# Optimization experiments

Measured on AMD Instinct MI355X. Metric: run time of the kernel, lower is better.

## Reference

```python
import jax, jax.numpy as jnp
import numpy as np

N, F, U = 32768, 512, 512
GRID_SIZE, SPLINE_ORDER = 3, 3
GRID_RANGE = (-1.0, 1.0)
LN_EPS = 1e-3  # keras LayerNormalization default epsilon


def _make_grid():
    h = (GRID_RANGE[1] - GRID_RANGE[0]) / GRID_SIZE
    start = -SPLINE_ORDER * h + GRID_RANGE[0]
    stop = (GRID_SIZE + SPLINE_ORDER) * h + GRID_RANGE[0]
    num = GRID_SIZE + 2 * SPLINE_ORDER + 1  # 10 knots
    g = np.linspace(start, stop, num, dtype=np.float32)
    g = np.tile(g, (F, 1))[None, :, :]  # [1, F, num]
    return jnp.asarray(g)


def _glorot(key, shape):
    limit = np.sqrt(6.0 / (shape[0] + shape[1])).astype(np.float32)
    return jax.random.uniform(key, shape, jnp.float32, -limit, limit)


def setup_inputs() -> dict:
    key = jax.random.key(0)
    k_x, k_bw, k_sw = jax.random.split(key, 3)
    return {
        "x": jax.random.normal(k_x, (N, F), jnp.float32),
        "ln_gamma": jnp.ones((F,), jnp.float32),
        "ln_beta": jnp.zeros((F,), jnp.float32),
        "base_weight": _glorot(k_bw, (F, U)),
        "base_bias": jnp.zeros((U,), jnp.float32),
        "spline_weight": _glorot(k_sw, (F * (GRID_SIZE + SPLINE_ORDER), U)),
        "grid": _make_grid(),
    }


def _b_splines(x, grid):
    # x: [N, F]; grid: [1, F, G+2K+1]
    xe = x[..., None]  # [N, F, 1]
    bases = ((xe >= grid[..., :-1]) & (xe < grid[..., 1:])).astype(x.dtype)  # [N,F,G+2K]
    for k in range(1, SPLINE_ORDER + 1):
        left = (xe - grid[..., :-(k + 1)]) / (grid[..., k:-1] - grid[..., :-(k + 1)])
        right = (grid[..., k + 1:] - xe) / (grid[..., k + 1:] - grid[..., 1:-k])
        bases = left * bases[..., :-1] + right * bases[..., 1:]
    return bases.reshape(x.shape[0], -1)  # [N, F*(G+K)]


def reference(x, ln_gamma, ln_beta, base_weight, base_bias, spline_weight, grid):
    # LayerNorm over last axis
    mean = jnp.mean(x, axis=-1, keepdims=True)
    var = jnp.var(x, axis=-1, keepdims=True)
    xn = (x - mean) * jax.lax.rsqrt(var + LN_EPS) * ln_gamma + ln_beta
    # base branch: relu -> matmul -> bias
    base_out = jax.nn.relu(xn) @ base_weight + base_bias
    # spline branch: Cox-de Boor basis -> matmul
    spline_out = _b_splines(xn, grid) @ spline_weight
    # dropout rate 0 / inference -> identity
    return base_out + spline_out
```

## Files before the change

### kernel.cpp

```cpp
#include <hip/hip_runtime.h>
#include <hip/hip_bf16.h>


#define N_ROWS 32768
#define F_DIM  512
#define U_DIM  512
#define K_DIM  4096

typedef short short8 __attribute__((ext_vector_type(8)));
typedef float floatx4 __attribute__((ext_vector_type(4)));

__device__ __forceinline__ float bf2f(unsigned short h) {
    return __uint_as_float(((unsigned int)h) << 16);
}
__device__ __forceinline__ bool probe_bf16(const void* grid) {
    return ((const unsigned int*)grid)[0] != 0xC0400000u;
}
template <bool B16>
__device__ __forceinline__ float ldf(const void* p, int i) {
    return B16 ? bf2f(((const unsigned short*)p)[i]) : ((const float*)p)[i];
}
template <bool B16>
__device__ __forceinline__ void ld4(const void* p, int i, float* o) {
    if (B16) {
        ushort4 v = *(const ushort4*)((const unsigned short*)p + i);
        o[0] = bf2f(v.x); o[1] = bf2f(v.y); o[2] = bf2f(v.z); o[3] = bf2f(v.w);
    } else {
        float4 v = *(const float4*)((const float*)p + i);
        o[0] = v.x; o[1] = v.y; o[2] = v.z; o[3] = v.w;
    }
}
__device__ __forceinline__ unsigned int pk2(float lo, float hi) {
    __hip_bfloat162 h = __float22bfloat162_rn(make_float2(lo, hi));
    return *reinterpret_cast<unsigned int*>(&h);
}

template <bool B16>
__device__ __forceinline__ void ln_stats_body(const void* __restrict__ x,
                                              float2* __restrict__ stats, int bid) {
    int wave = threadIdx.x >> 6, lane = threadIdx.x & 63;
    int row = bid * 4 + wave;
    float v[8];
    ld4<B16>(x, row * F_DIM + lane * 8, v);
    ld4<B16>(x, row * F_DIM + lane * 8 + 4, v + 4);
    float s = 0.f, s2 = 0.f;
#pragma unroll
    for (int k = 0; k < 8; ++k) { s += v[k]; s2 += v[k] * v[k]; }
#pragma unroll
    for (int off = 32; off > 0; off >>= 1) {
        s  += __shfl_xor(s, off);
        s2 += __shfl_xor(s2, off);
    }
    if (lane == 0) {
        float mean = s * (1.0f / F_DIM);
        float var  = s2 * (1.0f / F_DIM) - mean * mean;
        stats[row] = make_float2(mean, rsqrtf(var + 1e-3f));
    }
}
template <bool B16>
__device__ __forceinline__ void build_wt_body(const void* __restrict__ bw,
                                              const void* __restrict__ sw,
                                              unsigned short* __restrict__ wt, int bid) {
    int idx = bid * 256 + threadIdx.x;
    int u = idx & 511;
    int fq = idx >> 9;
#pragma unroll
    for (int i = 0; i < 4; ++i) {
        int f = fq * 4 + i;
        uint4 w;
        w.x = pk2(ldf<B16>(bw, f * U_DIM + u),            ldf<B16>(sw, (f * 6 + 0) * U_DIM + u));
        w.y = pk2(ldf<B16>(sw, (f * 6 + 1) * U_DIM + u),  ldf<B16>(sw, (f * 6 + 2) * U_DIM + u));
        w.z = pk2(ldf<B16>(sw, (f * 6 + 3) * U_DIM + u),  ldf<B16>(sw, (f * 6 + 4) * U_DIM + u));
        w.w = pk2(ldf<B16>(sw, (f * 6 + 5) * U_DIM + u),  0.f);
        *(uint4*)(wt + (size_t)u * K_DIM + f * 8) = w;
    }
}
__global__ __launch_bounds__(256) void prep_k(const void* __restrict__ x,
                                              const void* __restrict__ bw,
                                              const void* __restrict__ sw,
                                              const void* __restrict__ grid,
                                              float2* __restrict__ stats,
                                              unsigned short* __restrict__ wt) {
    int bid = blockIdx.x;
    if (probe_bf16(grid)) {
        if (bid < N_ROWS / 4) ln_stats_body<true>(x, stats, bid);
        else                  build_wt_body<true>(bw, sw, wt, bid - N_ROWS / 4);
    } else {
        if (bid < N_ROWS / 4) ln_stats_body<false>(x, stats, bid);
        else                  build_wt_body<false>(bw, sw, wt, bid - N_ROWS / 4);
    }
}

template <bool B16>
__device__ __forceinline__ uint4 gen_a_pack(const void* __restrict__ x,
                                            const void* __restrict__ gam,
                                            const void* __restrict__ bet,
                                            int xrow, int f, float mean, float rstd) {
    float xv = ldf<B16>(x, xrow + f);
    float gv = ldf<B16>(gam, f);
    float bv = ldf<B16>(bet, f);
    float xn = fmaf(xv - mean, rstd * gv, bv);
    float tt = fmaf(xn, 1.5f, 4.5f);
    float bb[6];
#pragma unroll
    for (int j = 0; j < 6; ++j) {
        float d = tt - (float)(j + 2);
        float a = fabsf(d);
        float a2 = d * d;
        float v1 = fmaf(fmaf(0.5f, a, -1.0f), a2, 0.66666669f);
        float c = fmaxf(2.0f - a, 0.0f);
        float v2 = c * c * c * (1.0f / 6.0f);
        bb[j] = (a < 1.0f) ? v1 : v2;
    }
    uint4 o;
    o.x = pk2(fmaxf(xn, 0.f), bb[0]);
    o.y = pk2(bb[1], bb[2]);
    o.z = pk2(bb[3], bb[4]);
    o.w = pk2(bb[5], 0.f);
    return o;
}

template <bool B16>
__device__ __forceinline__ void kan_gemm_body(
    const void* __restrict__ x,
    const float2* __restrict__ stats,
    const unsigned short* __restrict__ wt,
    const void* __restrict__ gam,
    const void* __restrict__ bet,
    const void* __restrict__ bias,
    void* __restrict__ out) {
    __shared__ __align__(16) unsigned short Alds[2][128 * 32];
    __shared__ __align__(16) unsigned short Blds[2][2048 * 8];

    const int tid = threadIdx.x;
    const int lane = tid & 63, wv = tid >> 6;
    const int rtile = blockIdx.x;

    const int arow = tid & 127, fg = tid >> 7;
    const int grow = rtile * 128 + arow;
    const float2 st = stats[grow];
    const float mean = st.x, rstd = st.y;
    const int xrow = grow * F_DIM;
    const int aslot = ((arow >> 4) * 4 + fg) * 16 + (arow & 15);

    const unsigned short* gsrc[4];
#pragma unroll
    for (int i = 0; i < 4; ++i) {
        int s = wv * 256 + i * 64 + lane;
        int C = ((s >> 6) << 4) | (s & 15);
        int q = (s >> 4) & 3;
        gsrc[i] = wt + (size_t)C * K_DIM + q * 8;
    }
    const int bbase = (wv * 256) * 8;

    const int wr = wv >> 2, wc = wv & 3;
    const int lr = lane & 15, lq = lane >> 4;

    floatx4 acc[4][8];
#pragma unroll
    for (int mi = 0; mi < 4; ++mi)
#pragma unroll
        for (int ni = 0; ni < 8; ++ni) acc[mi][ni] = (floatx4){0.f, 0.f, 0.f, 0.f};

#pragma unroll
    for (int i = 0; i < 4; ++i)
        __builtin_amdgcn_global_load_lds(
            (const __attribute__((address_space(1))) void*)gsrc[i],
            (__attribute__((address_space(3))) void*)&Blds[0][bbase + i * 64 * 8], 16, 0, 0);
    {
        uint4 p0 = gen_a_pack<B16>(x, gam, bet, xrow, fg, mean, rstd);
        *(uint4*)&Alds[0][aslot * 8] = p0;
    }
    __syncthreads();

    for (int ks = 0; ks < K_DIM / 32 - 1; ++ks) {
        const int cur = ks & 1, nxt = cur ^ 1;

#pragma unroll
        for (int i = 0; i < 4; ++i)
            __builtin_amdgcn_global_load_lds(
                (const __attribute__((address_space(1))) void*)(gsrc[i] + (ks + 1) * 32),
                (__attribute__((address_space(3))) void*)&Blds[nxt][bbase + i * 64 * 8], 16, 0, 0);

        short8 afr[4], bfr[8];
#pragma unroll
        for (int mi = 0; mi < 4; ++mi)
            afr[mi] = *(const short8*)&Alds[cur][((wr * 4 + mi) * 64 + lane) * 8];
#pragma unroll
        for (int ni = 0; ni < 8; ++ni)
            bfr[ni] = *(const short8*)&Blds[cur][((wc * 8 + ni) * 64 + lane) * 8];

        uint4 pkv = gen_a_pack<B16>(x, gam, bet, xrow, (ks + 1) * 4 + fg, mean, rstd);
        *(uint4*)&Alds[nxt][aslot * 8] = pkv;

#pragma unroll
        for (int mi = 0; mi < 4; ++mi)
#pragma unroll
            for (int ni = 0; ni < 8; ++ni)
                acc[mi][ni] = __builtin_amdgcn_mfma_f32_16x16x32_bf16(
                    afr[mi], bfr[ni], acc[mi][ni], 0, 0, 0);

        __syncthreads();
    }

    {
        short8 afr[4], bfr[8];
#pragma unroll
        for (int mi = 0; mi < 4; ++mi)
            afr[mi] = *(const short8*)&Alds[1][((wr * 4 + mi) * 64 + lane) * 8];
#pragma unroll
        for (int ni = 0; ni < 8; ++ni)
            bfr[ni] = *(const short8*)&Blds[1][((wc * 8 + ni) * 64 + lane) * 8];
#pragma unroll
        for (int mi = 0; mi < 4; ++mi)
#pragma unroll
            for (int ni = 0; ni < 8; ++ni)
                acc[mi][ni] = __builtin_amdgcn_mfma_f32_16x16x32_bf16(
                    afr[mi], bfr[ni], acc[mi][ni], 0, 0, 0);
    }

    float biasv[8];
#pragma unroll
    for (int ni = 0; ni < 8; ++ni)
        biasv[ni] = ldf<B16>(bias, wc * 128 + ni * 16 + lr);
#pragma unroll
    for (int mi = 0; mi < 4; ++mi)
#pragma unroll
        for (int ni = 0; ni < 8; ++ni)
#pragma unroll
            for (int r = 0; r < 4; ++r) {
                int row = rtile * 128 + wr * 64 + mi * 16 + lq * 4 + r;
                int col = wc * 128 + ni * 16 + lr;
                float val = acc[mi][ni][r] + biasv[ni];
                if (B16) ((unsigned short*)out)[(size_t)row * U_DIM + col] =
                    (unsigned short)(pk2(val, 0.f) & 0xffffu);
                else ((float*)out)[(size_t)row * U_DIM + col] = val;
            }
}
__global__ __launch_bounds__(512, 2) void kan_gemm(
    const void* __restrict__ x, const float2* __restrict__ stats,
    const unsigned short* __restrict__ wt, const void* __restrict__ gam,
    const void* __restrict__ bet, const void* __restrict__ bias,
    const void* __restrict__ grid, void* __restrict__ out) {
    if (probe_bf16(grid)) kan_gemm_body<true>(x, stats, wt, gam, bet, bias, out);
    else                  kan_gemm_body<false>(x, stats, wt, gam, bet, bias, out);
}

extern "C" void kernel_launch(void* const* d_in, const int* in_sizes, int n_in,
                              void* d_out, int out_size, void* d_ws, size_t ws_size,
                              hipStream_t stream) {
    const void* x    = d_in[0];
    const void* gam  = d_in[1];
    const void* bet  = d_in[2];
    const void* bw   = d_in[3];
    const void* bb   = d_in[4];
    const void* sw   = d_in[5];
    const void* grid = d_in[6];

    float2* stats = (float2*)d_ws;
    unsigned short* wt = (unsigned short*)((char*)d_ws + N_ROWS * sizeof(float2));

    hipLaunchKernelGGL(prep_k, dim3(N_ROWS / 4 + U_DIM * 128 / 256), dim3(256), 0, stream,
                       x, bw, sw, grid, stats, wt);
    hipLaunchKernelGGL(kan_gemm, dim3(N_ROWS / 128), dim3(512), 0, stream,
                       x, stats, wt, gam, bet, bb, grid, d_out);
}
```

Baseline: 356.2 us.

## Shrink GEMM row tile to 64 rows with 4 waves per block

Changes the fused LayerNorm/B-spline GEMM from a 128-row tile with 8 waves (2x4 wave grid) to a 64-row tile with 4 waves, each covering all 64 rows and 128 output columns. Each thread now loads 8 weight chunks per k-step instead of 4 and generates one A pack per k-step, keyed by its row and quad. The grid doubles to 512 blocks, which is meant to improve scheduling and fill across the GPU's compute units. In exchange, each weight tile is reused across half as many rows, so traffic for the 4 MB bf16 weight matrix doubles, and the per-block loads now fall on fewer threads.

Result: slower. 439.6 us (+23.4%).

```diff
diff --git a/kernel.cpp b/kernel.cpp
--- a/kernel.cpp
+++ b/kernel.cpp
@@ -128,32 +128,31 @@
     const void* __restrict__ gam,
     const void* __restrict__ bet,
     const void* __restrict__ bias,
-    void* __restrict__ out) {
-    __shared__ __align__(16) unsigned short Alds[2][128 * 32];
-    __shared__ __align__(16) unsigned short Blds[2][2048 * 8];
+    void* __restrict__ out,
+    unsigned short* __restrict__ Alds,
+    unsigned short* __restrict__ Blds) {
 
     const int tid = threadIdx.x;
     const int lane = tid & 63, wv = tid >> 6;
     const int rtile = blockIdx.x;
 
-    const int arow = tid & 127, fg = tid >> 7;
-    const int grow = rtile * 128 + arow;
+    const int ar = ((tid >> 6) << 4) | (tid & 15);
+    const int aq = (tid >> 4) & 3;
+    const int grow = rtile * 64 + ar;
     const float2 st = stats[grow];
     const float mean = st.x, rstd = st.y;
     const int xrow = grow * F_DIM;
-    const int aslot = ((arow >> 4) * 4 + fg) * 16 + (arow & 15);
-
-    const unsigned short* gsrc[4];
-#pragma unroll
-    for (int i = 0; i < 4; ++i) {
-        int s = wv * 256 + i * 64 + lane;
+
+    const unsigned short* gsrc[8];
+#pragma unroll
+    for (int i = 0; i < 8; ++i) {
+        int s = wv * 512 + i * 64 + lane;
         int C = ((s >> 6) << 4) | (s & 15);
         int q = (s >> 4) & 3;
         gsrc[i] = wt + (size_t)C * K_DIM + q * 8;
     }
-    const int bbase = (wv * 256) * 8;
-
-    const int wr = wv >> 2, wc = wv & 3;
+    const int bbase = wv * 512 * 8;
+
     const int lr = lane & 15, lq = lane >> 4;
 
     floatx4 acc[4][8];
@@ -163,35 +162,39 @@
         for (int ni = 0; ni < 8; ++ni) acc[mi][ni] = (floatx4){0.f, 0.f, 0.f, 0.f};
 
 #pragma unroll
-    for (int i = 0; i < 4; ++i)
+    for (int i = 0; i < 8; ++i)
         __builtin_amdgcn_global_load_lds(
             (const __attribute__((address_space(1))) void*)gsrc[i],
-            (__attribute__((address_space(3))) void*)&Blds[0][bbase + i * 64 * 8], 16, 0, 0);
+            (__attribute__((address_space(3))) void*)&Blds[bbase + i * 64 * 8], 16, 0, 0);
     {
-        uint4 p0 = gen_a_pack<B16>(x, gam, bet, xrow, fg, mean, rstd);
-        *(uint4*)&Alds[0][aslot * 8] = p0;
+        uint4 p0 = gen_a_pack<B16>(x, gam, bet, xrow, aq, mean, rstd);
+        *(uint4*)&Alds[tid * 8] = p0;
     }
     __syncthreads();
 
     for (int ks = 0; ks < K_DIM / 32 - 1; ++ks) {
         const int cur = ks & 1, nxt = cur ^ 1;
-
-#pragma unroll
-        for (int i = 0; i < 4; ++i)
+        unsigned short* __restrict__ Ac = Alds + cur * 2048;
+        unsigned short* __restrict__ An = Alds + nxt * 2048;
+        unsigned short* __restrict__ Bc = Blds + cur * 16384;
+        unsigned short* __restrict__ Bn = Blds + nxt * 16384;
+
+#pragma unroll
+        for (int i = 0; i < 8; ++i)
             __builtin_amdgcn_global_load_lds(
                 (const __attribute__((address_space(1))) void*)(gsrc[i] + (ks + 1) * 32),
-                (__attribute__((address_space(3))) void*)&Blds[nxt][bbase + i * 64 * 8], 16, 0, 0);
+                (__attribute__((address_space(3))) void*)&Bn[bbase + i * 64 * 8], 16, 0, 0);
 
         short8 afr[4], bfr[8];
 #pragma unroll
         for (int mi = 0; mi < 4; ++mi)
-            afr[mi] = *(const short8*)&Alds[cur][((wr * 4 + mi) * 64 + lane) * 8];
+            afr[mi] = *(const short8*)&Ac[(mi * 64 + lane) * 8];
 #pragma unroll
         for (int ni = 0; ni < 8; ++ni)
-            bfr[ni] = *(const short8*)&Blds[cur][((wc * 8 + ni) * 64 + lane) * 8];
-
-        uint4 pkv = gen_a_pack<B16>(x, gam, bet, xrow, (ks + 1) * 4 + fg, mean, rstd);
-        *(uint4*)&Alds[nxt][aslot * 8] = pkv;
+            bfr[ni] = *(const short8*)&Bc[((wv * 8 + ni) * 64 + lane) * 8];
+
+        uint4 pkv = gen_a_pack<B16>(x, gam, bet, xrow, (ks + 1) * 4 + aq, mean, rstd);
+        *(uint4*)&An[tid * 8] = pkv;
 
 #pragma unroll
         for (int mi = 0; mi < 4; ++mi)
@@ -204,13 +207,15 @@
     }
 
     {
+        const unsigned short* Ac = Alds + 2048;
+        const unsigned short* Bc = Blds + 16384;
         short8 afr[4], bfr[8];
 #pragma unroll
         for (int mi = 0; mi < 4; ++mi)
-            afr[mi] = *(const short8*)&Alds[1][((wr * 4 + mi) * 64 + lane) * 8];
+            afr[mi] = *(const short8*)&Ac[(mi * 64 + lane) * 8];
 #pragma unroll
         for (int ni = 0; ni < 8; ++ni)
-            bfr[ni] = *(const short8*)&Blds[1][((wc * 8 + ni) * 64 + lane) * 8];
+            bfr[ni] = *(const short8*)&Bc[((wv * 8 + ni) * 64 + lane) * 8];
 #pragma unroll
         for (int mi = 0; mi < 4; ++mi)
 #pragma unroll
@@ -222,28 +227,30 @@
     float biasv[8];
 #pragma unroll
     for (int ni = 0; ni < 8; ++ni)
-        biasv[ni] = ldf<B16>(bias, wc * 128 + ni * 16 + lr);
+        biasv[ni] = ldf<B16>(bias, wv * 128 + ni * 16 + lr);
 #pragma unroll
     for (int mi = 0; mi < 4; ++mi)
 #pragma unroll
         for (int ni = 0; ni < 8; ++ni)
 #pragma unroll
             for (int r = 0; r < 4; ++r) {
-                int row = rtile * 128 + wr * 64 + mi * 16 + lq * 4 + r;
-                int col = wc * 128 + ni * 16 + lr;
+                int row = rtile * 64 + mi * 16 + lq * 4 + r;
+                int col = wv * 128 + ni * 16 + lr;
                 float val = acc[mi][ni][r] + biasv[ni];
                 if (B16) ((unsigned short*)out)[(size_t)row * U_DIM + col] =
                     (unsigned short)(pk2(val, 0.f) & 0xffffu);
                 else ((float*)out)[(size_t)row * U_DIM + col] = val;
             }
 }
-__global__ __launch_bounds__(512, 2) void kan_gemm(
+__global__ __launch_bounds__(256, 2) void kan_gemm(
     const void* __restrict__ x, const float2* __restrict__ stats,
     const unsigned short* __restrict__ wt, const void* __restrict__ gam,
     const void* __restrict__ bet, const void* __restrict__ bias,
     const void* __restrict__ grid, void* __restrict__ out) {
-    if (probe_bf16(grid)) kan_gemm_body<true>(x, stats, wt, gam, bet, bias, out);
-    else                  kan_gemm_body<false>(x, stats, wt, gam, bet, bias, out);
+    __shared__ __align__(16) unsigned short Alds[2 * 2048];
+    __shared__ __align__(16) unsigned short Blds[2 * 16384];
+    if (probe_bf16(grid)) kan_gemm_body<true>(x, stats, wt, gam, bet, bias, out, Alds, Blds);
+    else                  kan_gemm_body<false>(x, stats, wt, gam, bet, bias, out, Alds, Blds);
 }
 
 extern "C" void kernel_launch(void* const* d_in, const int* in_sizes, int n_in,
@@ -262,6 +269,6 @@
 
     hipLaunchKernelGGL(prep_k, dim3(N_ROWS / 4 + U_DIM * 128 / 256), dim3(256), 0, stream,
                        x, bw, sw, grid, stats, wt);
-    hipLaunchKernelGGL(kan_gemm, dim3(N_ROWS / 128), dim3(512), 0, stream,
+    hipLaunchKernelGGL(kan_gemm, dim3(N_ROWS / 64), dim3(256), 0, stream,
                        x, stats, wt, gam, bet, bb, grid, d_out);
 }
```

## Fuse LayerNorm stats into GEMM, amortize A-tile generation across two k-steps

Applied to the files above, without the earlier changes.

Moves the per-row LayerNorm mean/rstd computation out of the prep kernel and into the GEMM block, which reduces each row tile from global memory before the main loop and keeps the stats in LDS. Gamma and beta are cached in LDS. The A tile now covers 8 features (two k-steps) per buffer, and the x values for future steps are prefetched into registers two groups ahead. MFMA sections are wrapped with s_setprio. This removes the stats round-trip through global memory and part of the prep launch work, at the cost of an extra read of x per block and more LDS use, which may lower occupancy.

New measurement: 331.7 us. 1.07x faster.

```diff
diff --git a/kernel.cpp b/kernel.cpp
--- a/kernel.cpp
+++ b/kernel.cpp
@@ -8,6 +8,7 @@
 #define K_DIM  4096
 
 typedef short short8 __attribute__((ext_vector_type(8)));
+typedef unsigned short ushort8v __attribute__((ext_vector_type(8)));
 typedef float floatx4 __attribute__((ext_vector_type(4)));
 
 __device__ __forceinline__ float bf2f(unsigned short h) {
@@ -21,42 +22,26 @@
     return B16 ? bf2f(((const unsigned short*)p)[i]) : ((const float*)p)[i];
 }
 template <bool B16>
-__device__ __forceinline__ void ld4(const void* p, int i, float* o) {
+__device__ __forceinline__ void ld8f(const void* p, int i, float* o) {
     if (B16) {
-        ushort4 v = *(const ushort4*)((const unsigned short*)p + i);
-        o[0] = bf2f(v.x); o[1] = bf2f(v.y); o[2] = bf2f(v.z); o[3] = bf2f(v.w);
+        ushort8v v = *(const ushort8v*)((const unsigned short*)p + i);
+#pragma unroll
+        for (int k = 0; k < 8; ++k) o[k] = bf2f(v[k]);
     } else {
-        float4 v = *(const float4*)((const float*)p + i);
-        o[0] = v.x; o[1] = v.y; o[2] = v.z; o[3] = v.w;
+        float4 a = *(const float4*)((const float*)p + i);
+        float4 b = *(const float4*)((const float*)p + i + 4);
+        o[0]=a.x; o[1]=a.y; o[2]=a.z; o[3]=a.w; o[4]=b.x; o[5]=b.y; o[6]=b.z; o[7]=b.w;
     }
 }
 __device__ __forceinline__ unsigned int pk2(float lo, float hi) {
     __hip_bfloat162 h = __float22bfloat162_rn(make_float2(lo, hi));
     return *reinterpret_cast<unsigned int*>(&h);
 }
-
-template <bool B16>
-__device__ __forceinline__ void ln_stats_body(const void* __restrict__ x,
-                                              float2* __restrict__ stats, int bid) {
-    int wave = threadIdx.x >> 6, lane = threadIdx.x & 63;
-    int row = bid * 4 + wave;
-    float v[8];
-    ld4<B16>(x, row * F_DIM + lane * 8, v);
-    ld4<B16>(x, row * F_DIM + lane * 8 + 4, v + 4);
-    float s = 0.f, s2 = 0.f;
-#pragma unroll
-    for (int k = 0; k < 8; ++k) { s += v[k]; s2 += v[k] * v[k]; }
-#pragma unroll
-    for (int off = 32; off > 0; off >>= 1) {
-        s  += __shfl_xor(s, off);
-        s2 += __shfl_xor(s2, off);
-    }
-    if (lane == 0) {
-        float mean = s * (1.0f / F_DIM);
-        float var  = s2 * (1.0f / F_DIM) - mean * mean;
-        stats[row] = make_float2(mean, rsqrtf(var + 1e-3f));
-    }
-}
+__device__ __forceinline__ void gld_lds16(const unsigned short* g, unsigned short* l) {
+    __builtin_amdgcn_global_load_lds((const __attribute__((address_space(1))) void*)g,
+                                     (__attribute__((address_space(3))) void*)l, 16, 0, 0);
+}
+
 template <bool B16>
 __device__ __forceinline__ void build_wt_body(const void* __restrict__ bw,
                                               const void* __restrict__ sw,
@@ -75,30 +60,16 @@
         *(uint4*)(wt + (size_t)u * K_DIM + f * 8) = w;
     }
 }
-__global__ __launch_bounds__(256) void prep_k(const void* __restrict__ x,
-                                              const void* __restrict__ bw,
+__global__ __launch_bounds__(256) void prep_k(const void* __restrict__ bw,
                                               const void* __restrict__ sw,
                                               const void* __restrict__ grid,
-                                              float2* __restrict__ stats,
                                               unsigned short* __restrict__ wt) {
-    int bid = blockIdx.x;
-    if (probe_bf16(grid)) {
-        if (bid < N_ROWS / 4) ln_stats_body<true>(x, stats, bid);
-        else                  build_wt_body<true>(bw, sw, wt, bid - N_ROWS / 4);
-    } else {
-        if (bid < N_ROWS / 4) ln_stats_body<false>(x, stats, bid);
-        else                  build_wt_body<false>(bw, sw, wt, bid - N_ROWS / 4);
-    }
-}
-
-template <bool B16>
-__device__ __forceinline__ uint4 gen_a_pack(const void* __restrict__ x,
-                                            const void* __restrict__ gam,
-                                            const void* __restrict__ bet,
-                                            int xrow, int f, float mean, float rstd) {
-    float xv = ldf<B16>(x, xrow + f);
-    float gv = ldf<B16>(gam, f);
-    float bv = ldf<B16>(bet, f);
+    if (probe_bf16(grid)) build_wt_body<true>(bw, sw, wt, blockIdx.x);
+    else                  build_wt_body<false>(bw, sw, wt, blockIdx.x);
+}
+
+__device__ __forceinline__ uint4 spline_pack(float xv, float gv, float bv,
+                                             float mean, float rstd) {
     float xn = fmaf(xv - mean, rstd * gv, bv);
     float tt = fmaf(xn, 1.5f, 4.5f);
     float bb[6];
@@ -123,25 +94,43 @@
 template <bool B16>
 __device__ __forceinline__ void kan_gemm_body(
     const void* __restrict__ x,
-    const float2* __restrict__ stats,
     const unsigned short* __restrict__ wt,
     const void* __restrict__ gam,
     const void* __restrict__ bet,
     const void* __restrict__ bias,
-    void* __restrict__ out) {
-    __shared__ __align__(16) unsigned short Alds[2][128 * 32];
-    __shared__ __align__(16) unsigned short Blds[2][2048 * 8];
+    void* __restrict__ out,
+    unsigned short* __restrict__ Alds,
+    unsigned short* __restrict__ Blds,
+    float2* __restrict__ gb,
+    float2* __restrict__ st) {
 
     const int tid = threadIdx.x;
     const int lane = tid & 63, wv = tid >> 6;
     const int rtile = blockIdx.x;
-
-    const int arow = tid & 127, fg = tid >> 7;
-    const int grow = rtile * 128 + arow;
-    const float2 st = stats[grow];
-    const float mean = st.x, rstd = st.y;
-    const int xrow = grow * F_DIM;
-    const int aslot = ((arow >> 4) * 4 + fg) * 16 + (arow & 15);
+    const int lr = lane & 15, lq = lane >> 4;
+    const int wr = wv >> 2, wc = wv & 3;
+
+    gb[tid] = make_float2(ldf<B16>(gam, tid), ldf<B16>(bet, tid));
+
+    {
+        const int row = tid >> 2, sub = tid & 3;
+        const int base = (rtile * 128 + row) * F_DIM + sub * 128;
+        float s = 0.f, s2 = 0.f;
+#pragma unroll
+        for (int i = 0; i < 16; ++i) {
+            float v[8];
+            ld8f<B16>(x, base + i * 8, v);
+#pragma unroll
+            for (int k = 0; k < 8; ++k) { s += v[k]; s2 += v[k] * v[k]; }
+        }
+        s += __shfl_xor(s, 1); s2 += __shfl_xor(s2, 1);
+        s += __shfl_xor(s, 2); s2 += __shfl_xor(s2, 2);
+        if (sub == 0) {
+            float mean = s * (1.0f / F_DIM);
+            float var  = s2 * (1.0f / F_DIM) - mean * mean;
+            st[row] = make_float2(mean, rsqrtf(var + 1e-3f));
+        }
+    }
 
     const unsigned short* gsrc[4];
 #pragma unroll
@@ -151,10 +140,37 @@
         int q = (s >> 4) & 3;
         gsrc[i] = wt + (size_t)C * K_DIM + q * 8;
     }
-    const int bbase = (wv * 256) * 8;
-
-    const int wr = wv >> 2, wc = wv & 3;
-    const int lr = lane & 15, lq = lane >> 4;
+#pragma unroll
+    for (int i = 0; i < 4; ++i)
+        gld_lds16(gsrc[i], &Blds[wv * 2048 + i * 512]);
+
+    __syncthreads();
+
+    const int ar = tid & 127, w = tid >> 7;
+    const float2 ms = st[ar];
+    const float mean = ms.x, rstd = ms.y;
+    const int xrow = (rtile * 128 + ar) * F_DIM;
+    const int aoff = (ar >> 4) * 512 + w * 128 + (ar & 15) * 8;
+
+    {
+        float x0 = ldf<B16>(x, xrow + w);
+        float x1 = ldf<B16>(x, xrow + 4 + w);
+        float2 ga = gb[w], gc = gb[4 + w];
+        *(uint4*)&Alds[aoff]        = spline_pack(x0, ga.x, ga.y, mean, rstd);
+        *(uint4*)&Alds[4096 + aoff] = spline_pack(x1, gc.x, gc.y, mean, rstd);
+    }
+    unsigned short xu0, xu1; float xf0, xf1;
+    if (B16) {
+        xu0 = ((const unsigned short*)x)[xrow + 8 + w];
+        xu1 = ((const unsigned short*)x)[xrow + 12 + w];
+    } else {
+        xf0 = ((const float*)x)[xrow + 8 + w];
+        xf1 = ((const float*)x)[xrow + 12 + w];
+    }
+    __syncthreads();
+    float xC[2];
+    if (B16) { xC[0] = bf2f(xu0); xC[1] = bf2f(xu1); }
+    else     { xC[0] = xf0;       xC[1] = xf1; }
 
     floatx4 acc[4][8];
 #pragma unroll
@@ -162,61 +178,57 @@
 #pragma unroll
         for (int ni = 0; ni < 8; ++ni) acc[mi][ni] = (floatx4){0.f, 0.f, 0.f, 0.f};
 
-#pragma unroll
-    for (int i = 0; i < 4; ++i)
-        __builtin_amdgcn_global_load_lds(
-            (const __attribute__((address_space(1))) void*)gsrc[i],
-            (__attribute__((address_space(3))) void*)&Blds[0][bbase + i * 64 * 8], 16, 0, 0);
-    {
-        uint4 p0 = gen_a_pack<B16>(x, gam, bet, xrow, fg, mean, rstd);
-        *(uint4*)&Alds[0][aslot * 8] = p0;
-    }
-    __syncthreads();
-
-    for (int ks = 0; ks < K_DIM / 32 - 1; ++ks) {
-        const int cur = ks & 1, nxt = cur ^ 1;
-
-#pragma unroll
-        for (int i = 0; i < 4; ++i)
-            __builtin_amdgcn_global_load_lds(
-                (const __attribute__((address_space(1))) void*)(gsrc[i] + (ks + 1) * 32),
-                (__attribute__((address_space(3))) void*)&Blds[nxt][bbase + i * 64 * 8], 16, 0, 0);
-
-        short8 afr[4], bfr[8];
-#pragma unroll
-        for (int mi = 0; mi < 4; ++mi)
-            afr[mi] = *(const short8*)&Alds[cur][((wr * 4 + mi) * 64 + lane) * 8];
-#pragma unroll
-        for (int ni = 0; ni < 8; ++ni)
-            bfr[ni] = *(const short8*)&Blds[cur][((wc * 8 + ni) * 64 + lane) * 8];
-
-        uint4 pkv = gen_a_pack<B16>(x, gam, bet, xrow, (ks + 1) * 4 + fg, mean, rstd);
-        *(uint4*)&Alds[nxt][aslot * 8] = pkv;
-
-#pragma unroll
-        for (int mi = 0; mi < 4; ++mi)
+    for (int g = 0; g < 64; ++g) {
+        unsigned short* __restrict__ Ac = Alds + (g & 1) * 8192;
+        unsigned short* __restrict__ An = Alds + ((g & 1) ^ 1) * 8192;
+        if (g < 62) {
+            int fx = (g + 2) * 8 + w;
+            if (B16) {
+                xu0 = ((const unsigned short*)x)[xrow + fx];
+                xu1 = ((const unsigned short*)x)[xrow + fx + 4];
+            } else {
+                xf0 = ((const float*)x)[xrow + fx];
+                xf1 = ((const float*)x)[xrow + fx + 4];
+            }
+        }
+        const bool dogen = (g < 63);
+        const int f0n = (g + 1) * 8 + w;
+#pragma unroll
+        for (int p = 0; p < 2; ++p) {
+            const int ks = g * 2 + p;
+            unsigned short* __restrict__ Bc = Blds + (ks & 1) * 16384;
+            unsigned short* __restrict__ Bn = Blds + ((ks & 1) ^ 1) * 16384;
+            if (ks < 127) {
+#pragma unroll
+                for (int i = 0; i < 4; ++i)
+                    gld_lds16(gsrc[i] + (ks + 1) * 32, &Bn[wv * 2048 + i * 512]);
+            }
+            short8 afr[4], bfr[8];
+#pragma unroll
+            for (int mi = 0; mi < 4; ++mi)
+                afr[mi] = *(const short8*)&Ac[p * 4096 + ((wr * 4 + mi) * 64 + lane) * 8];
 #pragma unroll
             for (int ni = 0; ni < 8; ++ni)
-                acc[mi][ni] = __builtin_amdgcn_mfma_f32_16x16x32_bf16(
-                    afr[mi], bfr[ni], acc[mi][ni], 0, 0, 0);
-
-        __syncthreads();
-    }
-
-    {
-        short8 afr[4], bfr[8];
-#pragma unroll
-        for (int mi = 0; mi < 4; ++mi)
-            afr[mi] = *(const short8*)&Alds[1][((wr * 4 + mi) * 64 + lane) * 8];
-#pragma unroll
-        for (int ni = 0; ni < 8; ++ni)
-            bfr[ni] = *(const short8*)&Blds[1][((wc * 8 + ni) * 64 + lane) * 8];
-#pragma unroll
-        for (int mi = 0; mi < 4; ++mi)
-#pragma unroll
-            for (int ni = 0; ni < 8; ++ni)
-                acc[mi][ni] = __builtin_amdgcn_mfma_f32_16x16x32_bf16(
-                    afr[mi], bfr[ni], acc[mi][ni], 0, 0, 0);
+                bfr[ni] = *(const short8*)&Bc[((wc * 8 + ni) * 64 + lane) * 8];
+            if (dogen) {
+                float2 g2 = gb[f0n + 4 * p];
+                *(uint4*)&An[p * 4096 + aoff] =
+                    spline_pack(xC[p], g2.x, g2.y, mean, rstd);
+            }
+            __builtin_amdgcn_s_setprio(1);
+#pragma unroll
+            for (int mi = 0; mi < 4; ++mi)
+#pragma unroll
+                for (int ni = 0; ni < 8; ++ni)
+                    acc[mi][ni] = __builtin_amdgcn_mfma_f32_16x16x32_bf16(
+                        afr[mi], bfr[ni], acc[mi][ni], 0, 0, 0);
+            __builtin_amdgcn_s_setprio(0);
+            __syncthreads();
+        }
+        if (g < 62) {
+            if (B16) { xC[0] = bf2f(xu0); xC[1] = bf2f(xu1); }
+            else     { xC[0] = xf0;       xC[1] = xf1; }
+        }
     }
 
     float biasv[8];
@@ -238,12 +250,18 @@
             }
 }
 __global__ __launch_bounds__(512, 2) void kan_gemm(
-    const void* __restrict__ x, const float2* __restrict__ stats,
-    const unsigned short* __restrict__ wt, const void* __restrict__ gam,
-    const void* __restrict__ bet, const void* __restrict__ bias,
-    const void* __restrict__ grid, void* __restrict__ out) {
-    if (probe_bf16(grid)) kan_gemm_body<true>(x, stats, wt, gam, bet, bias, out);
-    else                  kan_gemm_body<false>(x, stats, wt, gam, bet, bias, out);
+    const void* __restrict__ x, const unsigned short* __restrict__ wt,
+    const void* __restrict__ gam, const void* __restrict__ bet,
+    const void* __restrict__ bias, const void* __restrict__ grid,
+    void* __restrict__ out) {
+    __shared__ __align__(16) unsigned short Alds[2 * 8192];
+    __shared__ __align__(16) unsigned short Blds[2 * 16384];
+    __shared__ float2 gb_lds[512];
+    __shared__ float2 st_lds[128];
+    if (probe_bf16(grid))
+        kan_gemm_body<true>(x, wt, gam, bet, bias, out, Alds, Blds, gb_lds, st_lds);
+    else
+        kan_gemm_body<false>(x, wt, gam, bet, bias, out, Alds, Blds, gb_lds, st_lds);
 }
 
 extern "C" void kernel_launch(void* const* d_in, const int* in_sizes, int n_in,
@@ -257,11 +275,10 @@
     const void* sw   = d_in[5];
     const void* grid = d_in[6];
 
-    float2* stats = (float2*)d_ws;
-    unsigned short* wt = (unsigned short*)((char*)d_ws + N_ROWS * sizeof(float2));
-
-    hipLaunchKernelGGL(prep_k, dim3(N_ROWS / 4 + U_DIM * 128 / 256), dim3(256), 0, stream,
-                       x, bw, sw, grid, stats, wt);
+    unsigned short* wt = (unsigned short*)d_ws;
+
+    hipLaunchKernelGGL(prep_k, dim3(U_DIM * 128 / 256), dim3(256), 0, stream,
+                       bw, sw, grid, wt);
     hipLaunchKernelGGL(kan_gemm, dim3(N_ROWS / 128), dim3(512), 0, stream,
-                       x, stats, wt, gam, bet, bb, grid, d_out);
-}
+                       x, wt, gam, bet, bb, grid, d_out);
+}
```

## Split GEMM into 64x256 tiles with 2D grid, LDS gamma/beta, setprio

Applied to the files above, without the earlier changes.

Shrinks the per-block output tile from 128x512 to 64x256 using 256-thread blocks on a 2D grid, targeting three blocks per CU for more latency hiding. Gamma/beta are cached in LDS as float2 and MFMA sections are wrapped in s_setprio. The trade-off is duplicated spline basis generation across column tiles, more B-weight traffic, and fewer MFMAs per LDS fragment read.

Result: slower. 444.2 us (+24.7%).

```diff
diff --git a/kernel.cpp b/kernel.cpp
--- a/kernel.cpp
+++ b/kernel.cpp
@@ -8,6 +8,7 @@
 #define K_DIM  4096
 
 typedef short short8 __attribute__((ext_vector_type(8)));
+typedef unsigned short ushort8v __attribute__((ext_vector_type(8)));
 typedef float floatx4 __attribute__((ext_vector_type(4)));
 
 __device__ __forceinline__ float bf2f(unsigned short h) {
@@ -21,7 +22,7 @@
     return B16 ? bf2f(((const unsigned short*)p)[i]) : ((const float*)p)[i];
 }
 template <bool B16>
-__device__ __forceinline__ void ld4(const void* p, int i, float* o) {
+__device__ __forceinline__ void ld4v(const void* p, int i, float* o) {
     if (B16) {
         ushort4 v = *(const ushort4*)((const unsigned short*)p + i);
         o[0] = bf2f(v.x); o[1] = bf2f(v.y); o[2] = bf2f(v.z); o[3] = bf2f(v.w);
@@ -34,6 +35,10 @@
     __hip_bfloat162 h = __float22bfloat162_rn(make_float2(lo, hi));
     return *reinterpret_cast<unsigned int*>(&h);
 }
+__device__ __forceinline__ void gld_lds16(const unsigned short* g, unsigned short* l) {
+    __builtin_amdgcn_global_load_lds((const __attribute__((address_space(1))) void*)g,
+                                     (__attribute__((address_space(3))) void*)l, 16, 0, 0);
+}
 
 template <bool B16>
 __device__ __forceinline__ void ln_stats_body(const void* __restrict__ x,
@@ -41,8 +46,8 @@
     int wave = threadIdx.x >> 6, lane = threadIdx.x & 63;
     int row = bid * 4 + wave;
     float v[8];
-    ld4<B16>(x, row * F_DIM + lane * 8, v);
-    ld4<B16>(x, row * F_DIM + lane * 8 + 4, v + 4);
+    ld4v<B16>(x, row * F_DIM + lane * 8, v);
+    ld4v<B16>(x, row * F_DIM + lane * 8 + 4, v + 4);
     float s = 0.f, s2 = 0.f;
 #pragma unroll
     for (int k = 0; k < 8; ++k) { s += v[k]; s2 += v[k] * v[k]; }
@@ -91,14 +96,8 @@
     }
 }
 
-template <bool B16>
-__device__ __forceinline__ uint4 gen_a_pack(const void* __restrict__ x,
-                                            const void* __restrict__ gam,
-                                            const void* __restrict__ bet,
-                                            int xrow, int f, float mean, float rstd) {
-    float xv = ldf<B16>(x, xrow + f);
-    float gv = ldf<B16>(gam, f);
-    float bv = ldf<B16>(bet, f);
+__device__ __forceinline__ uint4 spline_pack(float xv, float gv, float bv,
+                                             float mean, float rstd) {
     float xn = fmaf(xv - mean, rstd * gv, bv);
     float tt = fmaf(xn, 1.5f, 4.5f);
     float bb[6];
@@ -128,20 +127,27 @@
     const void* __restrict__ gam,
     const void* __restrict__ bet,
     const void* __restrict__ bias,
-    void* __restrict__ out) {
-    __shared__ __align__(16) unsigned short Alds[2][128 * 32];
-    __shared__ __align__(16) unsigned short Blds[2][2048 * 8];
+    void* __restrict__ out,
+    unsigned short* __restrict__ Alds,
+    unsigned short* __restrict__ Blds,
+    float2* __restrict__ gb) {
 
     const int tid = threadIdx.x;
     const int lane = tid & 63, wv = tid >> 6;
-    const int rtile = blockIdx.x;
-
-    const int arow = tid & 127, fg = tid >> 7;
-    const int grow = rtile * 128 + arow;
+    const int ctile = blockIdx.x;
+    const int rtile = blockIdx.y;
+    const int lr = lane & 15, lq = lane >> 4;
+    const int wr = wv >> 1, wc = wv & 1;
+
+    gb[tid]       = make_float2(ldf<B16>(gam, tid),       ldf<B16>(bet, tid));
+    gb[tid + 256] = make_float2(ldf<B16>(gam, tid + 256), ldf<B16>(bet, tid + 256));
+
+    const int ar = tid >> 2, fg = tid & 3;
+    const int grow = rtile * 64 + ar;
     const float2 st = stats[grow];
     const float mean = st.x, rstd = st.y;
     const int xrow = grow * F_DIM;
-    const int aslot = ((arow >> 4) * 4 + fg) * 16 + (arow & 15);
+    const int aoff = (((ar >> 4) * 4 + fg) * 16 + (ar & 15)) * 8;
 
     const unsigned short* gsrc[4];
 #pragma unroll
@@ -149,70 +155,73 @@
         int s = wv * 256 + i * 64 + lane;
         int C = ((s >> 6) << 4) | (s & 15);
         int q = (s >> 4) & 3;
-        gsrc[i] = wt + (size_t)C * K_DIM + q * 8;
-    }
-    const int bbase = (wv * 256) * 8;
-
-    const int wr = wv >> 2, wc = wv & 3;
-    const int lr = lane & 15, lq = lane >> 4;
-
-    floatx4 acc[4][8];
-#pragma unroll
-    for (int mi = 0; mi < 4; ++mi)
+        gsrc[i] = wt + (size_t)(ctile * 256 + C) * K_DIM + q * 8;
+    }
+
+#pragma unroll
+    for (int i = 0; i < 4; ++i)
+        gld_lds16(gsrc[i], &Blds[(wv * 256 + i * 64) * 8]);
+    {
+        float xv = ldf<B16>(x, xrow + fg);
+        float gv = ldf<B16>(gam, fg), bv = ldf<B16>(bet, fg);
+        *(uint4*)&Alds[aoff] = spline_pack(xv, gv, bv, mean, rstd);
+    }
+    __syncthreads();
+
+    floatx4 acc[2][8];
+#pragma unroll
+    for (int mi = 0; mi < 2; ++mi)
 #pragma unroll
         for (int ni = 0; ni < 8; ++ni) acc[mi][ni] = (floatx4){0.f, 0.f, 0.f, 0.f};
-
-#pragma unroll
-    for (int i = 0; i < 4; ++i)
-        __builtin_amdgcn_global_load_lds(
-            (const __attribute__((address_space(1))) void*)gsrc[i],
-            (__attribute__((address_space(3))) void*)&Blds[0][bbase + i * 64 * 8], 16, 0, 0);
-    {
-        uint4 p0 = gen_a_pack<B16>(x, gam, bet, xrow, fg, mean, rstd);
-        *(uint4*)&Alds[0][aslot * 8] = p0;
-    }
-    __syncthreads();
 
     for (int ks = 0; ks < K_DIM / 32 - 1; ++ks) {
         const int cur = ks & 1, nxt = cur ^ 1;
+        const unsigned short* __restrict__ Ac = Alds + cur * 2048;
+        unsigned short* __restrict__ An = Alds + nxt * 2048;
+        const unsigned short* __restrict__ Bc = Blds + cur * 8192;
+        unsigned short* __restrict__ Bn = Blds + nxt * 8192;
 
 #pragma unroll
         for (int i = 0; i < 4; ++i)
-            __builtin_amdgcn_global_load_lds(
-                (const __attribute__((address_space(1))) void*)(gsrc[i] + (ks + 1) * 32),
-                (__attribute__((address_space(3))) void*)&Blds[nxt][bbase + i * 64 * 8], 16, 0, 0);
-
-        short8 afr[4], bfr[8];
-#pragma unroll
-        for (int mi = 0; mi < 4; ++mi)
-            afr[mi] = *(const short8*)&Alds[cur][((wr * 4 + mi) * 64 + lane) * 8];
+            gld_lds16(gsrc[i] + (ks + 1) * 32, &Bn[(wv * 256 + i * 64) * 8]);
+
+        short8 afr[2], bfr[8];
+#pragma unroll
+        for (int mi = 0; mi < 2; ++mi)
+            afr[mi] = *(const short8*)&Ac[((wr * 2 + mi) * 64 + lane) * 8];
 #pragma unroll
         for (int ni = 0; ni < 8; ++ni)
-            bfr[ni] = *(const short8*)&Blds[cur][((wc * 8 + ni) * 64 + lane) * 8];
-
-        uint4 pkv = gen_a_pack<B16>(x, gam, bet, xrow, (ks + 1) * 4 + fg, mean, rstd);
-        *(uint4*)&Alds[nxt][aslot * 8] = pkv;
-
-#pragma unroll
-        for (int mi = 0; mi < 4; ++mi)
+            bfr[ni] = *(const short8*)&Bc[((wc * 8 + ni) * 64 + lane) * 8];
+
+        {
+            float xv = ldf<B16>(x, xrow + (ks + 1) * 4 + fg);
+            float2 g2 = gb[(ks + 1) * 4 + fg];
+            *(uint4*)&An[aoff] = spline_pack(xv, g2.x, g2.y, mean, rstd);
+        }
+
+        __builtin_amdgcn_s_setprio(1);
+#pragma unroll
+        for (int mi = 0; mi < 2; ++mi)
 #pragma unroll
             for (int ni = 0; ni < 8; ++ni)
                 acc[mi][ni] = __builtin_amdgcn_mfma_f32_16x16x32_bf16(
                     afr[mi], bfr[ni], acc[mi][ni], 0, 0, 0);
-
+        __builtin_amdgcn_s_setprio(0);
         __syncthreads();
     }
 
     {
-        short8 afr[4], bfr[8];
-#pragma unroll
-        for (int mi = 0; mi < 4; ++mi)
-            afr[mi] = *(const short8*)&Alds[1][((wr * 4 + mi) * 64 + lane) * 8];
+        const unsigned short* Ac = Alds + 2048;
+        const unsigned short* Bc = Blds + 8192;
+        short8 afr[2], bfr[8];
+#pragma unroll
+        for (int mi = 0; mi < 2; ++mi)
+            afr[mi] = *(const short8*)&Ac[((wr * 2 + mi) * 64 + lane) * 8];
 #pragma unroll
         for (int ni = 0; ni < 8; ++ni)
-            bfr[ni] = *(const short8*)&Blds[1][((wc * 8 + ni) * 64 + lane) * 8];
-#pragma unroll
-        for (int mi = 0; mi < 4; ++mi)
+            bfr[ni] = *(const short8*)&Bc[((wc * 8 + ni) * 64 + lane) * 8];
+#pragma unroll
+        for (int mi = 0; mi < 2; ++mi)
 #pragma unroll
             for (int ni = 0; ni < 8; ++ni)
                 acc[mi][ni] = __builtin_amdgcn_mfma_f32_16x16x32_bf16(
@@ -222,28 +231,33 @@
     float biasv[8];
 #pragma unroll
     for (int ni = 0; ni < 8; ++ni)
-        biasv[ni] = ldf<B16>(bias, wc * 128 + ni * 16 + lr);
-#pragma unroll
-    for (int mi = 0; mi < 4; ++mi)
+        biasv[ni] = ldf<B16>(bias, ctile * 256 + wc * 128 + ni * 16 + lr);
+#pragma unroll
+    for (int mi = 0; mi < 2; ++mi)
 #pragma unroll
         for (int ni = 0; ni < 8; ++ni)
 #pragma unroll
             for (int r = 0; r < 4; ++r) {
-                int row = rtile * 128 + wr * 64 + mi * 16 + lq * 4 + r;
-                int col = wc * 128 + ni * 16 + lr;
+                int row = rtile * 64 + wr * 32 + mi * 16 + lq * 4 + r;
+                int col = ctile * 256 + wc * 128 + ni * 16 + lr;
                 float val = acc[mi][ni][r] + biasv[ni];
                 if (B16) ((unsigned short*)out)[(size_t)row * U_DIM + col] =
                     (unsigned short)(pk2(val, 0.f) & 0xffffu);
                 else ((float*)out)[(size_t)row * U_DIM + col] = val;
             }
 }
-__global__ __launch_bounds__(512, 2) void kan_gemm(
+__global__ __launch_bounds__(256, 3) void kan_gemm(
     const void* __restrict__ x, const float2* __restrict__ stats,
     const unsigned short* __restrict__ wt, const void* __restrict__ gam,
     const void* __restrict__ bet, const void* __restrict__ bias,
     const void* __restrict__ grid, void* __restrict__ out) {
-    if (probe_bf16(grid)) kan_gemm_body<true>(x, stats, wt, gam, bet, bias, out);
-    else                  kan_gemm_body<false>(x, stats, wt, gam, bet, bias, out);
+    __shared__ __align__(16) unsigned short Alds[2 * 2048];
+    __shared__ __align__(16) unsigned short Blds[2 * 8192];
+    __shared__ __align__(16) float2 gb_lds[512];
+    if (probe_bf16(grid))
+        kan_gemm_body<true>(x, stats, wt, gam, bet, bias, out, Alds, Blds, gb_lds);
+    else
+        kan_gemm_body<false>(x, stats, wt, gam, bet, bias, out, Alds, Blds, gb_lds);
 }
 
 extern "C" void kernel_launch(void* const* d_in, const int* in_sizes, int n_in,
@@ -262,6 +276,6 @@
 
     hipLaunchKernelGGL(prep_k, dim3(N_ROWS / 4 + U_DIM * 128 / 256), dim3(256), 0, stream,
                        x, bw, sw, grid, stats, wt);
-    hipLaunchKernelGGL(kan_gemm, dim3(N_ROWS / 128), dim3(512), 0, stream,
+    hipLaunchKernelGGL(kan_gemm, dim3(2, N_ROWS / 64), dim3(256), 0, stream,
                        x, stats, wt, gam, bet, bb, grid, d_out);
 }
```
